# Kernel tuning notes

Hardware: AMD Instinct MI355X
Metric: run time of the kernel (lower is better)

## Reference

```python
import jax, jax.numpy as jnp
import numpy as np

INIT_RANGE = 1e-4


def setup_inputs() -> dict:
    key = jax.random.key(0)
    k1, k2, k3, k4 = jax.random.split(key, 4)
    n, m = 2048, 2048
    K, p, q, r = 64, 32, 32, 1
    weights = jax.random.normal(k1, (n, m), dtype=jnp.float32)
    # uniform(-init_range, init_range) as in nn.init.uniform_
    pos_weights = jax.random.uniform(k2, (K, n // p, m // q), dtype=jnp.float32,
                                     minval=-INIT_RANGE, maxval=INIT_RANGE)
    # LowRankMatrix factors for the (K, p, q) prototypes
    proto_w = jax.random.normal(k3, (K, p, r), dtype=jnp.float32)
    proto_h = jax.random.normal(k4, (K, r, q), dtype=jnp.float32)
    return {"weights": weights, "pos_weights": pos_weights,
            "proto_w": proto_w, "proto_h": proto_h}


def reference(weights, pos_weights, proto_w, proto_h):
    # prototypes: (K, p, q) from low-rank factors
    protos = jnp.einsum('kpr,krq->kpq', proto_w, proto_h)
    K, I, J = pos_weights.shape          # I = n/p, J = m/q
    p, q = protos.shape[1], protos.shape[2]
    # sum_k kron(pos_weights[k], protos[k]):
    # delta[i*p+a, j*q+b] = sum_k pos[k,i,j] * proto[k,a,b]
    delta = jnp.einsum('kij,kab->iajb', pos_weights, protos).reshape(I * p, J * q)
    return weights + delta
```

## Files before the change

kernel.cpp:

```cpp
#include <hip/hip_runtime.h>


#define KDIM 64

__global__ __launch_bounds__(256) void splopa_kernel(
    const float* __restrict__ weights,
    const float* __restrict__ pos,
    const float* __restrict__ pw,
    const float* __restrict__ ph,
    float* __restrict__ out)
{
    __shared__ float w_lds[KDIM * 32];
    __shared__ float h_lds[KDIM * 32];

    const int tid = threadIdx.x;

    {
        const float4* wg = (const float4*)pw;
        const float4* hg = (const float4*)ph;
        float4* wl = (float4*)w_lds;
        float4* hl = (float4*)h_lds;
        wl[tid]       = wg[tid];
        wl[tid + 256] = wg[tid + 256];
        hl[tid]       = hg[tid];
        hl[tid + 256] = hg[tid + 256];
    }

    const int wave = tid >> 6;
    const int lane = tid & 63;

    const int t = (blockIdx.x << 2) + wave;
    const int i = t >> 6;
    const int j = t & 63;
    int ij = (i << 6) + j;
    ij = __builtin_amdgcn_readfirstlane(ij);

    const int a0 = (lane >> 3) << 2;
    const int b0 = (lane & 7) << 2;

    const int row0 = (i << 5) + a0;
    const int col0 = (j << 5) + b0;
    const float* wptr = weights + (size_t)row0 * 2048 + col0;
    float*       optr = out     + (size_t)row0 * 2048 + col0;

    float4 wt0 = *(const float4*)(wptr);
    float4 wt1 = *(const float4*)(wptr + 2048);
    float4 wt2 = *(const float4*)(wptr + 4096);
    float4 wt3 = *(const float4*)(wptr + 6144);

    float4 acc0 = {0.f, 0.f, 0.f, 0.f};
    float4 acc1 = {0.f, 0.f, 0.f, 0.f};
    float4 acc2 = {0.f, 0.f, 0.f, 0.f};
    float4 acc3 = {0.f, 0.f, 0.f, 0.f};

    __syncthreads();

    #pragma unroll
    for (int k = 0; k < KDIM; ++k) {
        const float  pk = pos[(k << 12) + ij];
        const float4 wv = *(const float4*)&w_lds[(k << 5) + a0];
        const float4 hv = *(const float4*)&h_lds[(k << 5) + b0];

        const float t0 = pk * wv.x;
        const float t1 = pk * wv.y;
        const float t2 = pk * wv.z;
        const float t3 = pk * wv.w;

        acc0.x += t0 * hv.x; acc0.y += t0 * hv.y; acc0.z += t0 * hv.z; acc0.w += t0 * hv.w;
        acc1.x += t1 * hv.x; acc1.y += t1 * hv.y; acc1.z += t1 * hv.z; acc1.w += t1 * hv.w;
        acc2.x += t2 * hv.x; acc2.y += t2 * hv.y; acc2.z += t2 * hv.z; acc2.w += t2 * hv.w;
        acc3.x += t3 * hv.x; acc3.y += t3 * hv.y; acc3.z += t3 * hv.z; acc3.w += t3 * hv.w;
    }

    wt0.x += acc0.x; wt0.y += acc0.y; wt0.z += acc0.z; wt0.w += acc0.w;
    wt1.x += acc1.x; wt1.y += acc1.y; wt1.z += acc1.z; wt1.w += acc1.w;
    wt2.x += acc2.x; wt2.y += acc2.y; wt2.z += acc2.z; wt2.w += acc2.w;
    wt3.x += acc3.x; wt3.y += acc3.y; wt3.z += acc3.z; wt3.w += acc3.w;

    *(float4*)(optr)        = wt0;
    *(float4*)(optr + 2048) = wt1;
    *(float4*)(optr + 4096) = wt2;
    *(float4*)(optr + 6144) = wt3;
}

extern "C" void kernel_launch(void* const* d_in, const int* in_sizes, int n_in,
                              void* d_out, int out_size, void* d_ws, size_t ws_size,
                              hipStream_t stream) {
    const float* weights = (const float*)d_in[0];
    const float* pos     = (const float*)d_in[1];
    const float* pw      = (const float*)d_in[2];
    const float* ph      = (const float*)d_in[3];
    float* out = (float*)d_out;

    splopa_kernel<<<1024, 256, 0, stream>>>(weights, pos, pw, ph, out);
}
```

Baseline: 80.57 us.

## Process four adjacent column tiles per wave to reuse LDS prototype loads

Each wave now computes four neighbouring 32x32 output tiles, not one. It loads four pos weights with one float4 read and reuses the prototype factor values read from LDS across all four tiles. Block size halves and the grid shrinks so total work coverage stays the same. This cuts LDS and scalar load traffic per output but lowers the wave count and raises register use, which may hurt latency hiding.

```diff
diff --git a/kernel.cpp b/kernel.cpp
--- a/kernel.cpp
+++ b/kernel.cpp
@@ -3,7 +3,7 @@
 
 #define KDIM 64
 
-__global__ __launch_bounds__(256) void splopa_kernel(
+__global__ __launch_bounds__(128) void splopa_kernel(
     const float* __restrict__ weights,
     const float* __restrict__ pos,
     const float* __restrict__ pw,
@@ -20,67 +20,81 @@
         const float4* hg = (const float4*)ph;
         float4* wl = (float4*)w_lds;
         float4* hl = (float4*)h_lds;
-        wl[tid]       = wg[tid];
-        wl[tid + 256] = wg[tid + 256];
-        hl[tid]       = hg[tid];
-        hl[tid + 256] = hg[tid + 256];
+        #pragma unroll
+        for (int it = 0; it < 4; ++it) {
+            wl[tid + 128 * it] = wg[tid + 128 * it];
+            hl[tid + 128 * it] = hg[tid + 128 * it];
+        }
     }
 
     const int wave = tid >> 6;
     const int lane = tid & 63;
 
-    const int t = (blockIdx.x << 2) + wave;
-    const int i = t >> 6;
-    const int j = t & 63;
-    int ij = (i << 6) + j;
+    const int t  = (blockIdx.x << 1) + wave;
+    const int i  = t >> 4;
+    const int j0 = (t & 15) << 2;
+    int ij = (i << 6) + j0;
     ij = __builtin_amdgcn_readfirstlane(ij);
 
     const int a0 = (lane >> 3) << 2;
     const int b0 = (lane & 7) << 2;
 
     const int row0 = (i << 5) + a0;
-    const int col0 = (j << 5) + b0;
+    const int col0 = (j0 << 5) + b0;
     const float* wptr = weights + (size_t)row0 * 2048 + col0;
     float*       optr = out     + (size_t)row0 * 2048 + col0;
 
-    float4 wt0 = *(const float4*)(wptr);
-    float4 wt1 = *(const float4*)(wptr + 2048);
-    float4 wt2 = *(const float4*)(wptr + 4096);
-    float4 wt3 = *(const float4*)(wptr + 6144);
+    float4 wt[4][4];
+    #pragma unroll
+    for (int tt = 0; tt < 4; ++tt)
+        #pragma unroll
+        for (int r = 0; r < 4; ++r)
+            wt[tt][r] = *(const float4*)(wptr + tt * 32 + (size_t)r * 2048);
 
-    float4 acc0 = {0.f, 0.f, 0.f, 0.f};
-    float4 acc1 = {0.f, 0.f, 0.f, 0.f};
-    float4 acc2 = {0.f, 0.f, 0.f, 0.f};
-    float4 acc3 = {0.f, 0.f, 0.f, 0.f};
+    float4 acc[4][4];
+    #pragma unroll
+    for (int tt = 0; tt < 4; ++tt)
+        #pragma unroll
+        for (int r = 0; r < 4; ++r)
+            acc[tt][r] = (float4){0.f, 0.f, 0.f, 0.f};
 
     __syncthreads();
 
-    #pragma unroll
+    #pragma unroll 8
     for (int k = 0; k < KDIM; ++k) {
-        const float  pk = pos[(k << 12) + ij];
+        const float4 pp = *(const float4*)&pos[(k << 12) + ij];
         const float4 wv = *(const float4*)&w_lds[(k << 5) + a0];
         const float4 hv = *(const float4*)&h_lds[(k << 5) + b0];
+        const float pk[4] = {pp.x, pp.y, pp.z, pp.w};
 
-        const float t0 = pk * wv.x;
-        const float t1 = pk * wv.y;
-        const float t2 = pk * wv.z;
-        const float t3 = pk * wv.w;
-
-        acc0.x += t0 * hv.x; acc0.y += t0 * hv.y; acc0.z += t0 * hv.z; acc0.w += t0 * hv.w;
-        acc1.x += t1 * hv.x; acc1.y += t1 * hv.y; acc1.z += t1 * hv.z; acc1.w += t1 * hv.w;
-        acc2.x += t2 * hv.x; acc2.y += t2 * hv.y; acc2.z += t2 * hv.z; acc2.w += t2 * hv.w;
-        acc3.x += t3 * hv.x; acc3.y += t3 * hv.y; acc3.z += t3 * hv.z; acc3.w += t3 * hv.w;
+        #pragma unroll
+        for (int tt = 0; tt < 4; ++tt) {
+            const float t0 = pk[tt] * wv.x;
+            const float t1 = pk[tt] * wv.y;
+            const float t2 = pk[tt] * wv.z;
+            const float t3 = pk[tt] * wv.w;
+            acc[tt][0].x += t0 * hv.x; acc[tt][0].y += t0 * hv.y;
+            acc[tt][0].z += t0 * hv.z; acc[tt][0].w += t0 * hv.w;
+            acc[tt][1].x += t1 * hv.x; acc[tt][1].y += t1 * hv.y;
+            acc[tt][1].z += t1 * hv.z; acc[tt][1].w += t1 * hv.w;
+            acc[tt][2].x += t2 * hv.x; acc[tt][2].y += t2 * hv.y;
+            acc[tt][2].z += t2 * hv.z; acc[tt][2].w += t2 * hv.w;
+            acc[tt][3].x += t3 * hv.x; acc[tt][3].y += t3 * hv.y;
+            acc[tt][3].z += t3 * hv.z; acc[tt][3].w += t3 * hv.w;
+        }
     }
 
-    wt0.x += acc0.x; wt0.y += acc0.y; wt0.z += acc0.z; wt0.w += acc0.w;
-    wt1.x += acc1.x; wt1.y += acc1.y; wt1.z += acc1.z; wt1.w += acc1.w;
-    wt2.x += acc2.x; wt2.y += acc2.y; wt2.z += acc2.z; wt2.w += acc2.w;
-    wt3.x += acc3.x; wt3.y += acc3.y; wt3.z += acc3.z; wt3.w += acc3.w;
-
-    *(float4*)(optr)        = wt0;
-    *(float4*)(optr + 2048) = wt1;
-    *(float4*)(optr + 4096) = wt2;
-    *(float4*)(optr + 6144) = wt3;
+    #pragma unroll
+    for (int tt = 0; tt < 4; ++tt) {
+        #pragma unroll
+        for (int r = 0; r < 4; ++r) {
+            wt[tt][r].x += acc[tt][r].x;
+            wt[tt][r].y += acc[tt][r].y;
+            wt[tt][r].z += acc[tt][r].z;
+            wt[tt][r].w += acc[tt][r].w;
+            *(float4*)(optr + tt * 32 + (size_t)r * 2048) = wt[tt][r];
+        }
+    }
 }
 
 extern "C" void kernel_launch(void* const* d_in, const int* in_sizes, int n_in,
@@ -92,5 +106,5 @@
     const float* ph      = (const float*)d_in[3];
     float* out = (float*)d_out;
 
-    splopa_kernel<<<1024, 256, 0, stream>>>(weights, pos, pw, ph, out);
+    splopa_kernel<<<512, 128, 0, stream>>>(weights, pos, pw, ph, out);
 }
```

After: 95.93 us. +19.1%, slower.
